# Performance work log

Hardware: AMD Instinct MI355X
Metric: run time of the kernel (lower is better)

## Reference

```python
import jax, jax.numpy as jnp
import numpy as np
from jax import lax

B, T_IN, T_OUT, U, V = 256, 512, 256, 256, 6


def setup_inputs() -> dict:
    key = jax.random.key(0)
    ks = jax.random.split(key, 12)
    s = lambda *sh: 0.05
    return {
        "ids": jax.random.randint(ks[0], (B, T_OUT), 0, V),
        "memory": jax.random.normal(ks[1], (B, T_IN, U), jnp.float32),
        "enc_h": jax.random.normal(ks[2], (B, U), jnp.float32),
        "enc_c": jax.random.normal(ks[3], (B, U), jnp.float32),
        "Wi": jax.random.normal(ks[4], (V + U, 4 * U), jnp.float32) * 0.05,
        "Wh": jax.random.normal(ks[5], (U, 4 * U), jnp.float32) * 0.05,
        "b": jnp.zeros((4 * U,), jnp.float32),
        "Wm": jax.random.normal(ks[6], (U, U), jnp.float32) * 0.05,
        "Wq": jax.random.normal(ks[7], (U, U), jnp.float32) * 0.05,
        "v": jax.random.normal(ks[8], (U,), jnp.float32) * 0.05,
        "Wa": jax.random.normal(ks[9], (2 * U, U), jnp.float32) * 0.05,
        "Wf": jax.random.normal(ks[10], (U, V), jnp.float32) * 0.05,
        "bf": jnp.zeros((V,), jnp.float32),
    }


def reference(ids, memory, enc_h, enc_c, Wi, Wh, b, Wm, Wq, v, Wa, Wf, bf):
    # Teacher-forcing BasicDecoder: AttentionWrapper(LSTMCell, BahdanauAttention) + Dense(vocab).
    vocab = Wf.shape[1]
    units = Wh.shape[0]
    # Bahdanau memory layer: processed keys, computed once.
    keys = jnp.einsum("bte,eu->btu", memory, Wm)  # [B, T_in, U]

    def step(carry, ids_t):
        h, c, attn = carry
        x = jax.nn.one_hot(ids_t, vocab, dtype=memory.dtype)  # one-hot 'embedding'
        cell_in = jnp.concatenate([x, attn], axis=-1)          # [B, V+U]
        z = cell_in @ Wi + h @ Wh + b                          # [B, 4U]
        i, f, g, o = jnp.split(z, 4, axis=-1)                  # keras gate order i,f,c,o
        c_new = jax.nn.sigmoid(f) * c + jax.nn.sigmoid(i) * jnp.tanh(g)
        h_new = jax.nn.sigmoid(o) * jnp.tanh(c_new)
        # Bahdanau additive attention, query = cell output
        pq = h_new @ Wq                                        # [B, U]
        score = jnp.einsum("btu,u->bt", jnp.tanh(keys + pq[:, None, :]), v)
        align = jax.nn.softmax(score, axis=-1)                 # full-length memory mask
        ctx = jnp.einsum("bt,bte->be", align, memory)
        attn_new = jnp.concatenate([h_new, ctx], axis=-1) @ Wa  # attention_layer (no bias)
        logits = attn_new @ Wf + bf
        return (h_new, c_new, attn_new), logits

    attn0 = jnp.zeros((enc_h.shape[0], units), memory.dtype)
    # TrainingSampler: decode T_out-1 steps, input at step t is ids[:, t]
    _, logits = lax.scan(step, (enc_h, enc_c, attn0), ids[:, :-1].T)
    return jnp.transpose(logits, (1, 0, 2))  # [B, T_out-1, vocab]
```

## Files before the change

### kernel.cpp

```cpp
#include <hip/hip_runtime.h>
#include <hip/hip_bf16.h>
#include <stdint.h>


typedef unsigned short u16;
typedef unsigned int u32;
typedef unsigned long long u64;
typedef short s16x8 __attribute__((ext_vector_type(8)));
typedef float f32x4 __attribute__((ext_vector_type(4)));

#define L2E 1.4426950408889634f

__device__ __forceinline__ u16 f2bf(float f) {
  u32 u = __float_as_uint(f);
  u += 0x7fffu + ((u >> 16) & 1u);
  return (u16)(u >> 16);
}
__device__ __forceinline__ float bflo(u32 p) { return __uint_as_float(p << 16); }
__device__ __forceinline__ float bfhi(u32 p) { return __uint_as_float(p & 0xffff0000u); }
__device__ __forceinline__ float b2f(u16 h) { return __uint_as_float(((u32)h) << 16); }

__device__ __forceinline__ float fast_sigmoid(float x) {
  float e = __builtin_amdgcn_exp2f(-x * L2E);
  return __builtin_amdgcn_rcpf(1.f + e);
}
__device__ __forceinline__ float fast_tanh(float x) {
  float e = __builtin_amdgcn_exp2f(x * (2.f * L2E));
  return fmaf(-2.f, __builtin_amdgcn_rcpf(e + 1.f), 1.f);
}

static const size_t OFF_KEYS = 0;
static const size_t OFF_MEMB = 67108864;
static const size_t OFF_WHC  = 134217728;
static const size_t OFF_W2   = 134742016;
static const size_t OFF_WHB  = 135266304;
static const size_t OFF_WQT  = 135790592;
static const size_t OFF_WMS  = 135921664;
static const size_t OFF_WFH  = 136052736;
static const size_t OFF_WFC  = 136058880;
static const size_t OFF_HB   = 136065024;
static const size_t OFF_CTX  = 136327168;
static const size_t OFF_BAR  = 136589312;

__device__ __forceinline__ void gbar(u32* bar, unsigned target) {
  __syncthreads();
  if (threadIdx.x == 0) {
    const unsigned want = (target << 4) - 1u;
    u32* gc = bar + ((blockIdx.x >> 4) << 5);
    unsigned pg = __hip_atomic_fetch_add(gc, 1u, __ATOMIC_RELAXED, __HIP_MEMORY_SCOPE_AGENT);
    if (pg == want) {
      unsigned pr = __hip_atomic_fetch_add(bar + 512, 1u, __ATOMIC_RELAXED, __HIP_MEMORY_SCOPE_AGENT);
      if (pr == want) {
        __hip_atomic_store(bar + 544, target, __ATOMIC_RELAXED, __HIP_MEMORY_SCOPE_AGENT);
      }
    }
    while (__hip_atomic_load(bar + 544, __ATOMIC_RELAXED, __HIP_MEMORY_SCOPE_AGENT) != target) {
      __builtin_amdgcn_s_sleep(1);
    }
  }
  __syncthreads();
}

__global__ __launch_bounds__(256) void k_cast(const float* __restrict__ src, u16* __restrict__ dst) {
  int i = blockIdx.x * 256 + threadIdx.x;
  const float4 f = *(const float4*)(src + (size_t)i * 4);
  ushort4 o;
  o.x = f2bf(f.x); o.y = f2bf(f.y); o.z = f2bf(f.z); o.w = f2bf(f.w);
  *(ushort4*)(dst + (size_t)i * 4) = o;
}

__global__ __launch_bounds__(256) void k_whc(const float* __restrict__ Wi, const float* __restrict__ Wh,
                                             const float* __restrict__ Wa, u16* __restrict__ WhCb,
                                             u16* __restrict__ W2b, u16* __restrict__ Whb) {
  int bl = blockIdx.x;
  int half = bl >> 10, r = (bl >> 2) & 255, cq = bl & 3;
  int c = cq * 256 + threadIdx.x;
  const float* war = Wa + (size_t)(half * 256 + r) * 256;
  float acc = 0.f;
#pragma unroll 4
  for (int a = 0; a < 256; ++a) acc = fmaf(war[a], Wi[(size_t)(6 + a) * 1024 + c], acc);
  if (half == 0) {
    float wh = Wh[(size_t)r * 1024 + c];
    WhCb[(size_t)r * 1024 + c] = f2bf(acc + wh);
    Whb[(size_t)r * 1024 + c] = f2bf(wh);
  } else {
    W2b[(size_t)r * 1024 + c] = f2bf(acc);
  }
}

__global__ __launch_bounds__(256) void k_wfhc(const float* __restrict__ Wa, const float* __restrict__ Wf,
                                              float* __restrict__ Wfh, float* __restrict__ Wfc) {
  int half = blockIdx.x, r = threadIdx.x;
  float acc[6] = {0.f, 0.f, 0.f, 0.f, 0.f, 0.f};
  const float* war = Wa + (size_t)(half * 256 + r) * 256;
  for (int a = 0; a < 256; ++a) {
    float w = war[a];
    const float* wfr = Wf + a * 6;
#pragma unroll
    for (int j = 0; j < 6; ++j) acc[j] = fmaf(w, wfr[j], acc[j]);
  }
  float* dst = half ? Wfc : Wfh;
#pragma unroll
  for (int j = 0; j < 6; ++j) dst[r * 6 + j] = acc[j];
}

__global__ __launch_bounds__(256) void k_wqt(const float* __restrict__ Wq, u16* __restrict__ WqT) {
  int g = blockIdx.x * 256 + threadIdx.x;
  int q = g >> 8, u = g & 255;
  WqT[q * 256 + u] = f2bf(Wq[u * 256 + q]);
}

__global__ __launch_bounds__(256) void k_wmswz(const float* __restrict__ Wm, u16* __restrict__ swz) {
  int g = blockIdx.x * 256 + threadIdx.x;
  int j = g & 7, n = (g >> 3) & 255, q = (g >> 11) & 3, i = g >> 13;
  swz[g] = f2bf(Wm[(32 * i + 8 * q + j) * 256 + n]);
}

__global__ __launch_bounds__(256) void k_init(const float* __restrict__ ench, u16* __restrict__ hbuf,
                                              u16* __restrict__ ctxbuf, u32* __restrict__ bar) {
  int b = blockIdx.x, tid = threadIdx.x;
  if (b == 256) {
    for (int i2 = tid; i2 < 576; i2 += 256) bar[i2] = 0u;
    return;
  }
  hbuf[b * 256 + tid] = f2bf(ench[b * 256 + tid]);
  ctxbuf[b * 256 + tid] = 0;
}

__global__ __launch_bounds__(256) void k_keys(const u16* __restrict__ memB, const u16* __restrict__ swz,
                                              u16* __restrict__ keysT) {
  int b = blockIdx.x >> 3, tt = blockIdx.x & 7;
  int w = threadIdx.x >> 6, lane = threadIdx.x & 63;
  int q = lane >> 4, mn = lane & 15;
  int t_load = tt * 64 + w * 16 + mn;
  const u16* arow = memB + ((size_t)b * 512 + t_load) * 256;
  s16x8 afr[8];
#pragma unroll
  for (int i = 0; i < 8; ++i) afr[i] = *(const s16x8*)(arow + 32 * i + 8 * q);
  for (int nt = 0; nt < 16; ++nt) {
    f32x4 acc = {0.f, 0.f, 0.f, 0.f};
#pragma unroll
    for (int i = 0; i < 8; ++i) {
      s16x8 bfr = *(const s16x8*)(swz + ((size_t)((i * 4 + q) * 256) + nt * 16 + mn) * 8);
      acc = __builtin_amdgcn_mfma_f32_16x16x32_bf16(afr[i], bfr, acc, 0, 0, 0);
    }
    int u = nt * 16 + mn;
    int tw = tt * 64 + w * 16 + q * 4;
    ushort4 kv;
    kv.x = f2bf(acc[0]); kv.y = f2bf(acc[1]); kv.z = f2bf(acc[2]); kv.w = f2bf(acc[3]);
    *(ushort4*)(keysT + ((size_t)b * 256 + u) * 512 + tw) = kv;
  }
}

struct ZScratch {
  u16 acts[16][520];
  float z4p[4][4][16][16];
};
struct AScratch {
  float h[256];
  float2 pqv[256];
  float qpart[4][256];
  float spart[4][512];
  float cpart[8][256];
  float align_[512];
  float ctx[256];
  float red[16];
};

__global__ __launch_bounds__(1024) void k_main(
    const int* __restrict__ ids, const float* __restrict__ encc, const float* __restrict__ Wi,
    const float* __restrict__ bvec, const float* __restrict__ vin, const float* __restrict__ bfv,
    const u16* __restrict__ WhCb, const u16* __restrict__ W2b, const u16* __restrict__ Whb,
    const u16* __restrict__ WqT, const u16* __restrict__ keysT, const u16* __restrict__ memB,
    const float* __restrict__ Wfh, const float* __restrict__ Wfc, u16* __restrict__ hbuf,
    u16* __restrict__ ctxbuf, u32* __restrict__ bar, float* __restrict__ out) {
  __shared__ __align__(16) union { ZScratch z; AScratch a; } smu;
  __shared__ __align__(16) u16 Wz[4][8192];
  __shared__ float Wx[6][64];
  __shared__ float bz[64];
  __shared__ float vsh[256];

  const int tid = threadIdx.x;
  const int bi = blockIdx.x >> 4, uj = blockIdx.x & 15;
  const int bb = blockIdx.x;

  if (tid < 256) vsh[tid] = vin[tid];
  if (tid < 384) {
    int id = tid >> 6, cl = tid & 63;
    Wx[id][cl] = Wi[(size_t)id * 1024 + 256 * (cl >> 4) + uj * 16 + (cl & 15)];
  }
  if (tid < 64) bz[tid] = bvec[256 * (tid >> 4) + uj * 16 + (tid & 15)];
  for (int ii = tid; ii < 32768; ii += 1024) {
    int g = ii >> 13, x2 = ii & 8191;
    int j = x2 & 7, n = (x2 >> 3) & 15, q2 = (x2 >> 7) & 3, i2 = x2 >> 9;
    int k = 32 * i2 + 8 * q2 + j;
    int col = 256 * g + uj * 16 + n;
    Wz[g][((i2 * 4 + q2) * 16 + n) * 8 + j] =
        (k < 256) ? Whb[(size_t)k * 1024 + col] : W2b[(size_t)(k - 256) * 1024 + col];
  }
  float creg = 0.f;
  if (tid < 256) creg = encc[(size_t)(bi * 16 + (tid >> 4)) * 256 + uj * 16 + (tid & 15)];
  unsigned ep = 0;
  __syncthreads();

  for (int t = 0; t < 255; ++t) {
    const int p = t & 1, p2 = p ^ 1;
    {
      const u16* hsrc = hbuf + p * 65536 + bi * 4096;
      const u16* csrc = ctxbuf + p * 65536 + bi * 4096;
#pragma unroll
      for (int k2 = 0; k2 < 2; ++k2) {
        int gidx = tid + k2 * 1024;
        int half = gidx >> 10, idx = gidx & 1023;
        int r = idx >> 6, c = idx & 63;
        const u16* srcp = (half ? csrc : hsrc) + r * 256 + c * 4;
        u64 val = __hip_atomic_load((const u64*)srcp, __ATOMIC_RELAXED, __HIP_MEMORY_SCOPE_AGENT);
        *(u64*)(&smu.z.acts[r][half * 256 + c * 4]) = val;
      }
      __syncthreads();
      {
        const int w = tid >> 6, lane = tid & 63, q = lane >> 4, mn = lane & 15;
        const int g = w & 3, kc = w >> 2;
        f32x4 acc = {0.f, 0.f, 0.f, 0.f};
#pragma unroll
        for (int ii2 = 0; ii2 < 4; ++ii2) {
          int i = kc * 4 + ii2;
          s16x8 af = *(const s16x8*)(&smu.z.acts[mn][32 * i + 8 * q]);
          s16x8 bvf = *(const s16x8*)(&Wz[g][((i * 4 + q) * 16 + mn) * 8]);
          acc = __builtin_amdgcn_mfma_f32_16x16x32_bf16(af, bvf, acc, 0, 0, 0);
        }
#pragma unroll
        for (int r2 = 0; r2 < 4; ++r2) smu.z.z4p[kc][g][q * 4 + r2][mn] = acc[r2];
      }
      __syncthreads();
      if (tid < 256) {
        const int b_l = tid >> 4, u_l = tid & 15;
        const int b_g = bi * 16 + b_l, u_g = uj * 16 + u_l;
        const int xid = ids[b_g * 256 + t];
        float zi = smu.z.z4p[0][0][b_l][u_l] + smu.z.z4p[1][0][b_l][u_l] +
                   smu.z.z4p[2][0][b_l][u_l] + smu.z.z4p[3][0][b_l][u_l] + Wx[xid][u_l] + bz[u_l];
        float zf = smu.z.z4p[0][1][b_l][u_l] + smu.z.z4p[1][1][b_l][u_l] +
                   smu.z.z4p[2][1][b_l][u_l] + smu.z.z4p[3][1][b_l][u_l] + Wx[xid][16 + u_l] + bz[16 + u_l];
        float zg = smu.z.z4p[0][2][b_l][u_l] + smu.z.z4p[1][2][b_l][u_l] +
                   smu.z.z4p[2][2][b_l][u_l] + smu.z.z4p[3][2][b_l][u_l] + Wx[xid][32 + u_l] + bz[32 + u_l];
        float zo = smu.z.z4p[0][3][b_l][u_l] + smu.z.z4p[1][3][b_l][u_l] +
                   smu.z.z4p[2][3][b_l][u_l] + smu.z.z4p[3][3][b_l][u_l] + Wx[xid][48 + u_l] + bz[48 + u_l];
        float gi = fast_sigmoid(zi), gf = fast_sigmoid(zf), go = fast_sigmoid(zo);
        creg = gf * creg + gi * fast_tanh(zg);
        float hn = go * fast_tanh(creg);
        u32 hb16 = f2bf(hn);
        u32 other = (u32)__shfl_xor((int)hb16, 1);
        if ((tid & 1) == 0) {
          __hip_atomic_store((u32*)(hbuf + p2 * 65536 + b_g * 256 + u_g), hb16 | (other << 16),
                             __ATOMIC_RELAXED, __HIP_MEMORY_SCOPE_AGENT);
        }
      }
      if (t == 0) {
        for (int ii3 = tid; ii3 < 16384; ii3 += 1024) {
          int g = ii3 >> 12, x2 = ii3 & 4095;
          int j = x2 & 7, n = (x2 >> 3) & 15, q2 = (x2 >> 7) & 3, i2 = (x2 >> 9) & 7;
          int k = 32 * i2 + 8 * q2 + j;
          Wz[g][((i2 * 4 + q2) * 16 + n) * 8 + j] = WhCb[(size_t)k * 1024 + 256 * g + uj * 16 + n];
        }
      }
    }
    gbar(bar, ++ep);
    {
      if (tid < 64) {
        const u16* hp = hbuf + p2 * 65536 + bb * 256 + tid * 4;
        u64 hv = __hip_atomic_load((const u64*)hp, __ATOMIC_RELAXED, __HIP_MEMORY_SCOPE_AGENT);
        smu.a.h[tid * 4 + 0] = b2f((u16)(hv));
        smu.a.h[tid * 4 + 1] = b2f((u16)(hv >> 16));
        smu.a.h[tid * 4 + 2] = b2f((u16)(hv >> 32));
        smu.a.h[tid * 4 + 3] = b2f((u16)(hv >> 48));
      }
      __syncthreads();
      {
        const int quarter = tid >> 8, qq = tid & 255;
        const u16* wqrow = WqT + qq * 256 + quarter * 64;
        const float* hq = &smu.a.h[quarter * 64];
        float pq = 0.f;
#pragma unroll
        for (int j = 0; j < 8; ++j) {
          uint4 wv = *(const uint4*)(wqrow + j * 8);
          pq = fmaf(bflo(wv.x), hq[j * 8 + 0], pq);
          pq = fmaf(bfhi(wv.x), hq[j * 8 + 1], pq);
          pq = fmaf(bflo(wv.y), hq[j * 8 + 2], pq);
          pq = fmaf(bfhi(wv.y), hq[j * 8 + 3], pq);
          pq = fmaf(bflo(wv.z), hq[j * 8 + 4], pq);
          pq = fmaf(bfhi(wv.z), hq[j * 8 + 5], pq);
          pq = fmaf(bflo(wv.w), hq[j * 8 + 6], pq);
          pq = fmaf(bfhi(wv.w), hq[j * 8 + 7], pq);
        }
        smu.a.qpart[quarter][qq] = pq;
      }
      __syncthreads();
      if (tid < 256) {
        float pq = smu.a.qpart[0][tid] + smu.a.qpart[1][tid] + smu.a.qpart[2][tid] + smu.a.qpart[3][tid];
        smu.a.pqv[tid] = make_float2(pq * (2.f * L2E), vsh[tid]);
      }
      __syncthreads();
      {
        const int ug = tid >> 8, tq = tid & 255;
        float s0 = 0.f, s1 = 0.f;
        const u16* kbase = keysT + (size_t)bb * 131072 + 2 * tq;
#pragma unroll 8
        for (int u = ug * 64; u < ug * 64 + 64; ++u) {
          u32 kk = *(const u32*)(kbase + (size_t)u * 512);
          float2 pv = smu.a.pqv[u];
          float a0 = fmaf(bflo(kk), 2.f * L2E, pv.x);
          float a1 = fmaf(bfhi(kk), 2.f * L2E, pv.x);
          float r0 = __builtin_amdgcn_rcpf(__builtin_amdgcn_exp2f(a0) + 1.f);
          float r1 = __builtin_amdgcn_rcpf(__builtin_amdgcn_exp2f(a1) + 1.f);
          s0 = fmaf(fmaf(-2.f, r0, 1.f), pv.y, s0);
          s1 = fmaf(fmaf(-2.f, r1, 1.f), pv.y, s1);
        }
        smu.a.spart[ug][2 * tq] = s0;
        smu.a.spart[ug][2 * tq + 1] = s1;
      }
      __syncthreads();
      float sc = 0.f, e = 0.f;
      if (tid < 512) {
        sc = smu.a.spart[0][tid] + smu.a.spart[1][tid] + smu.a.spart[2][tid] + smu.a.spart[3][tid];
        float mx = sc;
#pragma unroll
        for (int o = 32; o >= 1; o >>= 1) mx = fmaxf(mx, __shfl_xor(mx, o));
        if ((tid & 63) == 0) smu.a.red[tid >> 6] = mx;
      }
      __syncthreads();
      if (tid < 512) {
        float M = smu.a.red[0];
#pragma unroll
        for (int k = 1; k < 8; ++k) M = fmaxf(M, smu.a.red[k]);
        e = __builtin_amdgcn_exp2f((sc - M) * L2E);
        float ss = e;
#pragma unroll
        for (int o = 32; o >= 1; o >>= 1) ss += __shfl_xor(ss, o);
        if ((tid & 63) == 0) smu.a.red[8 + (tid >> 6)] = ss;
      }
      __syncthreads();
      if (tid < 512) {
        float S = 0.f;
#pragma unroll
        for (int k = 0; k < 8; ++k) S += smu.a.red[8 + k];
        smu.a.align_[tid] = e * __builtin_amdgcn_rcpf(S);
      }
      __syncthreads();
      {
        const int tg = tid >> 7, up = (tid & 127) * 2;
        float c0 = 0.f, c1 = 0.f;
        const u16* mbase = memB + (size_t)bb * 131072 + (size_t)tg * 16384 + up;
#pragma unroll 8
        for (int i = 0; i < 64; ++i) {
          u32 mm = *(const u32*)(mbase + (size_t)i * 256);
          float al = smu.a.align_[tg * 64 + i];
          c0 = fmaf(al, bflo(mm), c0);
          c1 = fmaf(al, bfhi(mm), c1);
        }
        smu.a.cpart[tg][up] = c0;
        smu.a.cpart[tg][up + 1] = c1;
      }
      __syncthreads();
      if (tid < 256) {
        float cv = 0.f;
#pragma unroll
        for (int k = 0; k < 8; ++k) cv += smu.a.cpart[k][tid];
        smu.a.ctx[tid] = cv;
        u32 cb16 = f2bf(cv);
        u32 oth = (u32)__shfl_xor((int)cb16, 1);
        if ((tid & 1) == 0) {
          __hip_atomic_store((u32*)(ctxbuf + p2 * 65536 + bb * 256 + tid), cb16 | (oth << 16),
                             __ATOMIC_RELAXED, __HIP_MEMORY_SCOPE_AGENT);
        }
      }
      __syncthreads();
      if (tid < 384) {
        const int jj = tid >> 6, l = tid & 63;
        float acc2 = 0.f;
#pragma unroll
        for (int u = l; u < 256; u += 64)
          acc2 += smu.a.h[u] * Wfh[u * 6 + jj] + smu.a.ctx[u] * Wfc[u * 6 + jj];
#pragma unroll
        for (int o = 32; o >= 1; o >>= 1) acc2 += __shfl_down(acc2, o);
        if (l == 0) out[((size_t)bb * 255 + t) * 6 + jj] = acc2 + bfv[jj];
      }
    }
    gbar(bar, ++ep);
  }
}

extern "C" void kernel_launch(void* const* d_in, const int* in_sizes, int n_in,
                              void* d_out, int out_size, void* d_ws, size_t ws_size,
                              hipStream_t stream) {
  const int* ids = (const int*)d_in[0];
  const float* mem = (const float*)d_in[1];
  const float* ench = (const float*)d_in[2];
  const float* encc = (const float*)d_in[3];
  const float* Wi = (const float*)d_in[4];
  const float* Wh = (const float*)d_in[5];
  const float* bv = (const float*)d_in[6];
  const float* Wm = (const float*)d_in[7];
  const float* Wq = (const float*)d_in[8];
  const float* vv = (const float*)d_in[9];
  const float* Wa = (const float*)d_in[10];
  const float* Wf = (const float*)d_in[11];
  const float* bf = (const float*)d_in[12];
  float* out = (float*)d_out;

  char* ws = (char*)d_ws;
  u16* keysT = (u16*)(ws + OFF_KEYS);
  u16* memB = (u16*)(ws + OFF_MEMB);
  u16* whcb = (u16*)(ws + OFF_WHC);
  u16* w2b = (u16*)(ws + OFF_W2);
  u16* whb = (u16*)(ws + OFF_WHB);
  u16* wqt = (u16*)(ws + OFF_WQT);
  u16* wms = (u16*)(ws + OFF_WMS);
  float* wfh = (float*)(ws + OFF_WFH);
  float* wfc = (float*)(ws + OFF_WFC);
  u16* hb = (u16*)(ws + OFF_HB);
  u16* cb = (u16*)(ws + OFF_CTX);
  u32* bar = (u32*)(ws + OFF_BAR);

  hipLaunchKernelGGL(k_cast, dim3(32768), dim3(256), 0, stream, mem, memB);
  hipLaunchKernelGGL(k_whc, dim3(2048), dim3(256), 0, stream, Wi, Wh, Wa, whcb, w2b, whb);
  hipLaunchKernelGGL(k_wfhc, dim3(2), dim3(256), 0, stream, Wa, Wf, wfh, wfc);
  hipLaunchKernelGGL(k_wqt, dim3(256), dim3(256), 0, stream, Wq, wqt);
  hipLaunchKernelGGL(k_wmswz, dim3(256), dim3(256), 0, stream, Wm, wms);
  hipLaunchKernelGGL(k_init, dim3(257), dim3(256), 0, stream, ench, hb, cb, bar);
  hipLaunchKernelGGL(k_keys, dim3(2048), dim3(256), 0, stream, memB, wms, keysT);
  hipLaunchKernelGGL(k_main, dim3(256), dim3(1024), 0, stream, ids, encc, Wi, bv, vv, bf,
                     whcb, w2b, whb, wqt, keysT, memB, wfh, wfc, hb, cb, bar, out);
}
```

Before: 11.47 ms.

## Store keys and memory in fp8, group-local barrier, drop softmax max pass

Processed attention keys and the memory tensor are now stored as fp8 instead of bf16, which halves the per-step bytes streamed in the score and context loops. The loops are rewritten to unpack four fp8 values per load with nontemporal hints. The global two-level barrier becomes a barrier local to each 16-block batch group. Softmax now skips the max subtraction and applies normalization after the context sum, removing two block syncs per step. The trade-offs are lower precision, possible overflow in the exponent since the max is no longer subtracted, and a barrier change that relies on only intra-group dependencies.

```diff
diff --git a/kernel.cpp b/kernel.cpp
--- a/kernel.cpp
+++ b/kernel.cpp
@@ -3,11 +3,13 @@
 #include <stdint.h>
 
 
+typedef unsigned char u8;
 typedef unsigned short u16;
 typedef unsigned int u32;
 typedef unsigned long long u64;
 typedef short s16x8 __attribute__((ext_vector_type(8)));
 typedef float f32x4 __attribute__((ext_vector_type(4)));
+typedef float f32x2 __attribute__((ext_vector_type(2)));
 
 #define L2E 1.4426950408889634f
 
@@ -29,7 +31,8 @@
   return fmaf(-2.f, __builtin_amdgcn_rcpf(e + 1.f), 1.f);
 }
 
-static const size_t OFF_KEYS = 0;
+static const size_t OFF_K8   = 0;
+static const size_t OFF_M8   = 33554432;
 static const size_t OFF_MEMB = 67108864;
 static const size_t OFF_WHC  = 134217728;
 static const size_t OFF_W2   = 134742016;
@@ -42,31 +45,27 @@
 static const size_t OFF_CTX  = 136327168;
 static const size_t OFF_BAR  = 136589312;
 
-__device__ __forceinline__ void gbar(u32* bar, unsigned target) {
+__device__ __forceinline__ void grpbar(u32* gc, unsigned target) {
   __syncthreads();
   if (threadIdx.x == 0) {
-    const unsigned want = (target << 4) - 1u;
-    u32* gc = bar + ((blockIdx.x >> 4) << 5);
-    unsigned pg = __hip_atomic_fetch_add(gc, 1u, __ATOMIC_RELAXED, __HIP_MEMORY_SCOPE_AGENT);
-    if (pg == want) {
-      unsigned pr = __hip_atomic_fetch_add(bar + 512, 1u, __ATOMIC_RELAXED, __HIP_MEMORY_SCOPE_AGENT);
-      if (pr == want) {
-        __hip_atomic_store(bar + 544, target, __ATOMIC_RELAXED, __HIP_MEMORY_SCOPE_AGENT);
-      }
-    }
-    while (__hip_atomic_load(bar + 544, __ATOMIC_RELAXED, __HIP_MEMORY_SCOPE_AGENT) != target) {
+    __hip_atomic_fetch_add(gc, 1u, __ATOMIC_RELAXED, __HIP_MEMORY_SCOPE_AGENT);
+    while (__hip_atomic_load(gc, __ATOMIC_RELAXED, __HIP_MEMORY_SCOPE_AGENT) < target) {
       __builtin_amdgcn_s_sleep(1);
     }
   }
   __syncthreads();
 }
 
-__global__ __launch_bounds__(256) void k_cast(const float* __restrict__ src, u16* __restrict__ dst) {
+__global__ __launch_bounds__(256) void k_cast(const float* __restrict__ src, u16* __restrict__ dstb,
+                                              u32* __restrict__ dst8) {
   int i = blockIdx.x * 256 + threadIdx.x;
   const float4 f = *(const float4*)(src + (size_t)i * 4);
   ushort4 o;
   o.x = f2bf(f.x); o.y = f2bf(f.y); o.z = f2bf(f.z); o.w = f2bf(f.w);
-  *(ushort4*)(dst + (size_t)i * 4) = o;
+  *(ushort4*)(dstb + (size_t)i * 4) = o;
+  int p8 = __builtin_amdgcn_cvt_pk_fp8_f32(f.x, f.y, 0, false);
+  p8 = __builtin_amdgcn_cvt_pk_fp8_f32(f.z, f.w, p8, true);
+  dst8[i] = (u32)p8;
 }
 
 __global__ __launch_bounds__(256) void k_whc(const float* __restrict__ Wi, const float* __restrict__ Wh,
@@ -120,7 +119,7 @@
                                               u16* __restrict__ ctxbuf, u32* __restrict__ bar) {
   int b = blockIdx.x, tid = threadIdx.x;
   if (b == 256) {
-    for (int i2 = tid; i2 < 576; i2 += 256) bar[i2] = 0u;
+    for (int i = tid; i < 512; i += 256) bar[i] = 0u;
     return;
   }
   hbuf[b * 256 + tid] = f2bf(ench[b * 256 + tid]);
@@ -128,7 +127,7 @@
 }
 
 __global__ __launch_bounds__(256) void k_keys(const u16* __restrict__ memB, const u16* __restrict__ swz,
-                                              u16* __restrict__ keysT) {
+                                              u32* __restrict__ keys8) {
   int b = blockIdx.x >> 3, tt = blockIdx.x & 7;
   int w = threadIdx.x >> 6, lane = threadIdx.x & 63;
   int q = lane >> 4, mn = lane & 15;
@@ -146,9 +145,9 @@
     }
     int u = nt * 16 + mn;
     int tw = tt * 64 + w * 16 + q * 4;
-    ushort4 kv;
-    kv.x = f2bf(acc[0]); kv.y = f2bf(acc[1]); kv.z = f2bf(acc[2]); kv.w = f2bf(acc[3]);
-    *(ushort4*)(keysT + ((size_t)b * 256 + u) * 512 + tw) = kv;
+    int p8 = __builtin_amdgcn_cvt_pk_fp8_f32(acc[0], acc[1], 0, false);
+    p8 = __builtin_amdgcn_cvt_pk_fp8_f32(acc[2], acc[3], p8, true);
+    keys8[((size_t)b * 256 + u) * 128 + (tw >> 2)] = (u32)p8;
   }
 }
 
@@ -158,20 +157,20 @@
 };
 struct AScratch {
   float h[256];
-  float2 pqv[256];
+  f32x2 pqv[256];
   float qpart[4][256];
-  float spart[4][512];
-  float cpart[8][256];
-  float align_[512];
+  float spart[8][512];
+  float esh[512];
+  float cpart[16][256];
   float ctx[256];
-  float red[16];
+  float red[8];
 };
 
 __global__ __launch_bounds__(1024) void k_main(
     const int* __restrict__ ids, const float* __restrict__ encc, const float* __restrict__ Wi,
     const float* __restrict__ bvec, const float* __restrict__ vin, const float* __restrict__ bfv,
     const u16* __restrict__ WhCb, const u16* __restrict__ W2b, const u16* __restrict__ Whb,
-    const u16* __restrict__ WqT, const u16* __restrict__ keysT, const u16* __restrict__ memB,
+    const u16* __restrict__ WqT, const u8* __restrict__ keys8, const u8* __restrict__ mem8,
     const float* __restrict__ Wfh, const float* __restrict__ Wfc, u16* __restrict__ hbuf,
     u16* __restrict__ ctxbuf, u32* __restrict__ bar, float* __restrict__ out) {
   __shared__ __align__(16) union { ZScratch z; AScratch a; } smu;
@@ -183,6 +182,7 @@
   const int tid = threadIdx.x;
   const int bi = blockIdx.x >> 4, uj = blockIdx.x & 15;
   const int bb = blockIdx.x;
+  u32* gc = bar + ((bb >> 4) << 5);
 
   if (tid < 256) vsh[tid] = vin[tid];
   if (tid < 384) {
@@ -264,7 +264,7 @@
         }
       }
     }
-    gbar(bar, ++ep);
+    grpbar(gc, (++ep) << 4);
     {
       if (tid < 64) {
         const u16* hp = hbuf + p2 * 65536 + bb * 256 + tid * 4;
@@ -297,78 +297,81 @@
       __syncthreads();
       if (tid < 256) {
         float pq = smu.a.qpart[0][tid] + smu.a.qpart[1][tid] + smu.a.qpart[2][tid] + smu.a.qpart[3][tid];
-        smu.a.pqv[tid] = make_float2(pq * (2.f * L2E), vsh[tid]);
+        f32x2 pv; pv.x = pq * (2.f * L2E); pv.y = vsh[tid];
+        smu.a.pqv[tid] = pv;
       }
       __syncthreads();
       {
-        const int ug = tid >> 8, tq = tid & 255;
-        float s0 = 0.f, s1 = 0.f;
-        const u16* kbase = keysT + (size_t)bb * 131072 + 2 * tq;
-#pragma unroll 8
-        for (int u = ug * 64; u < ug * 64 + 64; ++u) {
-          u32 kk = *(const u32*)(kbase + (size_t)u * 512);
-          float2 pv = smu.a.pqv[u];
-          float a0 = fmaf(bflo(kk), 2.f * L2E, pv.x);
-          float a1 = fmaf(bfhi(kk), 2.f * L2E, pv.x);
+        const int ug = tid >> 7, tq = tid & 127;
+        float s0 = 0.f, s1 = 0.f, s2 = 0.f, s3 = 0.f;
+        const u32* kb = (const u32*)(keys8 + (size_t)bb * 131072) + tq;
+#pragma unroll 4
+        for (int u = ug * 32; u < ug * 32 + 32; ++u) {
+          u32 kk = __builtin_nontemporal_load(kb + u * 128);
+          f32x2 pv = smu.a.pqv[u];
+          f32x2 lo = __builtin_amdgcn_cvt_pk_f32_fp8(kk, false);
+          f32x2 hi = __builtin_amdgcn_cvt_pk_f32_fp8(kk, true);
+          float a0 = fmaf(lo.x, 2.f * L2E, pv.x);
+          float a1 = fmaf(lo.y, 2.f * L2E, pv.x);
+          float a2 = fmaf(hi.x, 2.f * L2E, pv.x);
+          float a3 = fmaf(hi.y, 2.f * L2E, pv.x);
           float r0 = __builtin_amdgcn_rcpf(__builtin_amdgcn_exp2f(a0) + 1.f);
           float r1 = __builtin_amdgcn_rcpf(__builtin_amdgcn_exp2f(a1) + 1.f);
+          float r2 = __builtin_amdgcn_rcpf(__builtin_amdgcn_exp2f(a2) + 1.f);
+          float r3 = __builtin_amdgcn_rcpf(__builtin_amdgcn_exp2f(a3) + 1.f);
           s0 = fmaf(fmaf(-2.f, r0, 1.f), pv.y, s0);
           s1 = fmaf(fmaf(-2.f, r1, 1.f), pv.y, s1);
-        }
-        smu.a.spart[ug][2 * tq] = s0;
-        smu.a.spart[ug][2 * tq + 1] = s1;
-      }
-      __syncthreads();
-      float sc = 0.f, e = 0.f;
+          s2 = fmaf(fmaf(-2.f, r2, 1.f), pv.y, s2);
+          s3 = fmaf(fmaf(-2.f, r3, 1.f), pv.y, s3);
+        }
+        float4 sv; sv.x = s0; sv.y = s1; sv.z = s2; sv.w = s3;
+        *(float4*)&smu.a.spart[ug][4 * tq] = sv;
+      }
+      __syncthreads();
       if (tid < 512) {
-        sc = smu.a.spart[0][tid] + smu.a.spart[1][tid] + smu.a.spart[2][tid] + smu.a.spart[3][tid];
-        float mx = sc;
-#pragma unroll
-        for (int o = 32; o >= 1; o >>= 1) mx = fmaxf(mx, __shfl_xor(mx, o));
-        if ((tid & 63) == 0) smu.a.red[tid >> 6] = mx;
-      }
-      __syncthreads();
-      if (tid < 512) {
-        float M = smu.a.red[0];
-#pragma unroll
-        for (int k = 1; k < 8; ++k) M = fmaxf(M, smu.a.red[k]);
-        e = __builtin_amdgcn_exp2f((sc - M) * L2E);
+        float sc = smu.a.spart[0][tid] + smu.a.spart[1][tid] + smu.a.spart[2][tid] +
+                   smu.a.spart[3][tid] + smu.a.spart[4][tid] + smu.a.spart[5][tid] +
+                   smu.a.spart[6][tid] + smu.a.spart[7][tid];
+        float e = __builtin_amdgcn_exp2f(sc * L2E);
+        smu.a.esh[tid] = e;
         float ss = e;
 #pragma unroll
         for (int o = 32; o >= 1; o >>= 1) ss += __shfl_xor(ss, o);
-        if ((tid & 63) == 0) smu.a.red[8 + (tid >> 6)] = ss;
-      }
-      __syncthreads();
-      if (tid < 512) {
-        float S = 0.f;
-#pragma unroll
-        for (int k = 0; k < 8; ++k) S += smu.a.red[8 + k];
-        smu.a.align_[tid] = e * __builtin_amdgcn_rcpf(S);
+        if ((tid & 63) == 0) smu.a.red[tid >> 6] = ss;
       }
       __syncthreads();
       {
-        const int tg = tid >> 7, up = (tid & 127) * 2;
-        float c0 = 0.f, c1 = 0.f;
-        const u16* mbase = memB + (size_t)bb * 131072 + (size_t)tg * 16384 + up;
-#pragma unroll 8
-        for (int i = 0; i < 64; ++i) {
-          u32 mm = *(const u32*)(mbase + (size_t)i * 256);
-          float al = smu.a.align_[tg * 64 + i];
-          c0 = fmaf(al, bflo(mm), c0);
-          c1 = fmaf(al, bfhi(mm), c1);
-        }
-        smu.a.cpart[tg][up] = c0;
-        smu.a.cpart[tg][up + 1] = c1;
+        const int tg = tid >> 6, uq = tid & 63;
+        float c0 = 0.f, c1 = 0.f, c2 = 0.f, c3 = 0.f;
+        const u32* mb = (const u32*)(mem8 + (size_t)bb * 131072) + uq;
+#pragma unroll 4
+        for (int i = 0; i < 32; ++i) {
+          int tt2 = tg * 32 + i;
+          u32 mm = __builtin_nontemporal_load(mb + tt2 * 64);
+          float e = smu.a.esh[tt2];
+          f32x2 lo = __builtin_amdgcn_cvt_pk_f32_fp8(mm, false);
+          f32x2 hi = __builtin_amdgcn_cvt_pk_f32_fp8(mm, true);
+          c0 = fmaf(e, lo.x, c0);
+          c1 = fmaf(e, lo.y, c1);
+          c2 = fmaf(e, hi.x, c2);
+          c3 = fmaf(e, hi.y, c3);
+        }
+        float4 cv4; cv4.x = c0; cv4.y = c1; cv4.z = c2; cv4.w = c3;
+        *(float4*)&smu.a.cpart[tg][4 * uq] = cv4;
       }
       __syncthreads();
       if (tid < 256) {
+        float S = (smu.a.red[0] + smu.a.red[1]) + (smu.a.red[2] + smu.a.red[3]) +
+                  (smu.a.red[4] + smu.a.red[5]) + (smu.a.red[6] + smu.a.red[7]);
+        float rs = __builtin_amdgcn_rcpf(S);
         float cv = 0.f;
 #pragma unroll
-        for (int k = 0; k < 8; ++k) cv += smu.a.cpart[k][tid];
+        for (int k = 0; k < 16; ++k) cv += smu.a.cpart[k][tid];
+        cv *= rs;
         smu.a.ctx[tid] = cv;
         u32 cb16 = f2bf(cv);
         u32 oth = (u32)__shfl_xor((int)cb16, 1);
-        if ((tid & 1) == 0) {
+        if (!(tid & 1)) {
           __hip_atomic_store((u32*)(ctxbuf + p2 * 65536 + bb * 256 + tid), cb16 | (oth << 16),
                              __ATOMIC_RELAXED, __HIP_MEMORY_SCOPE_AGENT);
         }
@@ -385,7 +388,7 @@
         if (l == 0) out[((size_t)bb * 255 + t) * 6 + jj] = acc2 + bfv[jj];
       }
     }
-    gbar(bar, ++ep);
+    grpbar(gc, (++ep) << 4);
   }
 }
 
@@ -408,7 +411,8 @@
   float* out = (float*)d_out;
 
   char* ws = (char*)d_ws;
-  u16* keysT = (u16*)(ws + OFF_KEYS);
+  u8* keys8 = (u8*)(ws + OFF_K8);
+  u8* mem8 = (u8*)(ws + OFF_M8);
   u16* memB = (u16*)(ws + OFF_MEMB);
   u16* whcb = (u16*)(ws + OFF_WHC);
   u16* w2b = (u16*)(ws + OFF_W2);
@@ -421,13 +425,13 @@
   u16* cb = (u16*)(ws + OFF_CTX);
   u32* bar = (u32*)(ws + OFF_BAR);
 
-  hipLaunchKernelGGL(k_cast, dim3(32768), dim3(256), 0, stream, mem, memB);
+  hipLaunchKernelGGL(k_cast, dim3(32768), dim3(256), 0, stream, mem, memB, (u32*)mem8);
   hipLaunchKernelGGL(k_whc, dim3(2048), dim3(256), 0, stream, Wi, Wh, Wa, whcb, w2b, whb);
   hipLaunchKernelGGL(k_wfhc, dim3(2), dim3(256), 0, stream, Wa, Wf, wfh, wfc);
   hipLaunchKernelGGL(k_wqt, dim3(256), dim3(256), 0, stream, Wq, wqt);
   hipLaunchKernelGGL(k_wmswz, dim3(256), dim3(256), 0, stream, Wm, wms);
   hipLaunchKernelGGL(k_init, dim3(257), dim3(256), 0, stream, ench, hb, cb, bar);
-  hipLaunchKernelGGL(k_keys, dim3(2048), dim3(256), 0, stream, memB, wms, keysT);
+  hipLaunchKernelGGL(k_keys, dim3(2048), dim3(256), 0, stream, memB, wms, (u32*)keys8);
   hipLaunchKernelGGL(k_main, dim3(256), dim3(1024), 0, stream, ids, encc, Wi, bv, vv, bf,
-                     whcb, w2b, whb, wqt, keysT, memB, wfh, wfc, hb, cb, bar, out);
-}
+                     whcb, w2b, whb, wqt, keys8, mem8, wfh, wfc, hb, cb, bar, out);
+}
```

After: 10.33 ms. 10.0% less time.
